# Kernel tuning notes

Hardware: AMD Instinct MI355X
Metric: run time of the kernel (lower is better)

The kernel has to match this reference:

```python
import jax, jax.numpy as jnp
import numpy as np

V, E, H, B, T = 32000, 256, 256, 4, 512


def setup_inputs() -> dict:
    key = jax.random.key(0)
    ks = jax.random.split(key, 16)
    s = 0.02
    d = {
        "x": jax.random.randint(ks[0], (B, T), 0, V, dtype=jnp.int64 if jax.config.read('jax_enable_x64') else jnp.int32).astype(jnp.int32),
        "h": jnp.zeros((1, B, H), jnp.float32),
        "embed_W": jax.random.normal(ks[1], (V, E), jnp.float32) * s,
        "gru_w_ih": jax.random.normal(ks[2], (3 * H, E), jnp.float32) * s,
        "gru_b_ih": jnp.zeros((3 * H,), jnp.float32),
        "gru_w_hh": jax.random.normal(ks[3], (3 * H, H), jnp.float32) * s,
        "gru_b_hh": jnp.zeros((3 * H,), jnp.float32),
        "attn_w_W": jax.random.normal(ks[4], (H, H), jnp.float32) * s,
        "attn_w_b": jnp.zeros((H,), jnp.float32),
        "attn_u_W": jax.random.normal(ks[5], (H, H), jnp.float32) * s,
        "attn_u_b": jnp.zeros((H,), jnp.float32),
        "attn_v_W": jax.random.normal(ks[6], (1, H), jnp.float32) * s,
        "attn_v_b": jnp.zeros((1,), jnp.float32),
        "fc_W": jax.random.normal(ks[7], (V, 2 * H), jnp.float32) * s,
        "fc_b": jnp.zeros((V,), jnp.float32),
    }
    return d


def reference(x, h, embed_W, gru_w_ih, gru_b_ih, gru_w_hh, gru_b_hh,
              attn_w_W, attn_w_b, attn_u_W, attn_u_b, attn_v_W, attn_v_b,
              fc_W, fc_b):
    # Embedding (dropout is identity in eval mode)
    emb = embed_W[x]                                   # [B,T,E]
    # GRU (single layer, batch_first), PyTorch gate math
    xp = emb @ gru_w_ih.T + gru_b_ih                   # [B,T,3H]
    h0 = h[0]                                          # [B,H]

    def step(hc, xpt):
        hp = hc @ gru_w_hh.T + gru_b_hh
        xr, xz, xn = jnp.split(xpt, 3, axis=-1)
        hr, hz, hn = jnp.split(hp, 3, axis=-1)
        r = jax.nn.sigmoid(xr + hr)
        z = jax.nn.sigmoid(xz + hz)
        n = jnp.tanh(xn + r * hn)
        h_new = (1.0 - z) * n + z * hc
        return h_new, h_new

    h_last, outs = jax.lax.scan(step, h0, jnp.swapaxes(xp, 0, 1))
    out = jnp.swapaxes(outs, 0, 1)                     # [B,T,H]

    # Bahdanau additive attention with causal mask
    q = out @ attn_w_W.T + attn_w_b                    # [B,T,H]
    k = out @ attn_u_W.T + attn_u_b                    # [B,T,H]
    e = jnp.tanh(q[:, :, None, :] + k[:, None, :, :])  # [B,T,T,H] (big intermediate)
    scores = jnp.einsum('bijh,h->bij', e, attn_v_W[0]) + attn_v_b[0]
    Tq = scores.shape[-1]
    causal_mask = jnp.triu(jnp.ones((Tq, Tq), bool), k=1)
    scores = jnp.where(causal_mask, -jnp.inf, scores)
    attn = jax.nn.softmax(scores, axis=-1)             # [B,T,T]
    ctx = jnp.einsum('bij,bjh->bih', attn, out)        # [B,T,H]

    combined = jnp.concatenate([out, ctx], axis=-1)    # [B,T,2H]
    logits = combined @ fc_W.T + fc_b                  # [B,T,V]
    return logits, h_last[None]
```

## Files before the change

kernel.cpp:

```cpp
#include <hip/hip_runtime.h>
#include <cstdint>
#include <cstddef>

#define Vv 32000
#define Ee 256
#define Hh 256
#define Bb 4
#define Tt 512
#define Mm (Bb*Tt)

typedef unsigned int u32;
typedef unsigned short u16;
typedef unsigned long long u64;
typedef __bf16 bf16x8 __attribute__((ext_vector_type(8)));
typedef float f32x4 __attribute__((ext_vector_type(4)));

__device__ __forceinline__ u16 f2bf(float f) {
  u32 u = __float_as_uint(f);
  u32 r = (u + 0x7FFFu + ((u >> 16) & 1u)) >> 16;
  return (u16)r;
}

template<bool GATHER>
__global__ __launch_bounds__(256) void gemm_small(
    const float* __restrict__ A, const int* __restrict__ xidx,
    const float* __restrict__ W, const float* __restrict__ bias,
    float* __restrict__ C, int N)
{
  __shared__ float At[64][36];
  __shared__ float Wt[64][66];
  const int tid = threadIdx.x;
  const int m0 = blockIdx.x * 32;
  const int n0 = blockIdx.y * 64;
  const int tm = tid >> 5;
  const int tn = tid & 31;
  float acc[4][2] = {};

  for (int k0 = 0; k0 < 256; k0 += 64) {
    __syncthreads();
    #pragma unroll
    for (int r = 0; r < 2; ++r) {
      int idx = tid + r*256;
      int i  = idx >> 4;
      int c4 = idx & 15;
      const float* src;
      if (GATHER) src = A + (size_t)xidx[m0+i]*256 + k0 + c4*4;
      else        src = A + (size_t)(m0+i)*256 + k0 + c4*4;
      float4 v = *(const float4*)src;
      At[c4*4+0][i]=v.x; At[c4*4+1][i]=v.y; At[c4*4+2][i]=v.z; At[c4*4+3][i]=v.w;
    }
    #pragma unroll
    for (int r = 0; r < 4; ++r) {
      int idx = tid + r*256;
      int j  = idx >> 4;
      int c4 = idx & 15;
      float4 v = *(const float4*)(W + (size_t)(n0+j)*256 + k0 + c4*4);
      Wt[c4*4+0][j]=v.x; Wt[c4*4+1][j]=v.y; Wt[c4*4+2][j]=v.z; Wt[c4*4+3][j]=v.w;
    }
    __syncthreads();
    #pragma unroll 8
    for (int k = 0; k < 64; ++k) {
      float4 a = *(const float4*)&At[k][tm*4];
      float2 w = *(const float2*)&Wt[k][tn*2];
      acc[0][0] += a.x*w.x; acc[0][1] += a.x*w.y;
      acc[1][0] += a.y*w.x; acc[1][1] += a.y*w.y;
      acc[2][0] += a.z*w.x; acc[2][1] += a.z*w.y;
      acc[3][0] += a.w*w.x; acc[3][1] += a.w*w.y;
    }
  }
  #pragma unroll
  for (int i = 0; i < 4; ++i)
    #pragma unroll
    for (int j = 0; j < 2; ++j) {
      int m = m0 + tm*4 + i, n = n0 + tn*2 + j;
      C[(size_t)m*N + n] = acc[i][j] + bias[n];
    }
}

__global__ __launch_bounds__(192, 1) void gru_scan(
    const float* __restrict__ xp, const float* __restrict__ h0,
    const float* __restrict__ whh, const float* __restrict__ bhh,
    float* __restrict__ gout, u64* __restrict__ hpair,
    const float* __restrict__ fcW, u16* __restrict__ Wb)
{
  const int tid = threadIdx.x;
  const int bid = blockIdx.x;
  const int b = bid & 7;
  const int c = bid >> 3;

  if (b >= 4) {
    const int cbid = (c << 2) | (b - 4);
    const int n8 = Vv*512/8;
    for (int i = cbid*192 + tid; i < n8; i += 32*192) {
      float4 a = ((const float4*)fcW)[i*2];
      float4 v = ((const float4*)fcW)[i*2+1];
      uint4 o;
      o.x = (u32)f2bf(a.x) | ((u32)f2bf(a.y) << 16);
      o.y = (u32)f2bf(a.z) | ((u32)f2bf(a.w) << 16);
      o.z = (u32)f2bf(v.x) | ((u32)f2bf(v.y) << 16);
      o.w = (u32)f2bf(v.z) | ((u32)f2bf(v.w) << 16);
      ((uint4*)Wb)[i] = o;
    }
    return;
  }

  __shared__ __attribute__((aligned(16))) float hl[256];
  __shared__ float dl[96];

  const int r = tid >> 1;
  const int q = tid & 1;
  const int grow = (r >> 5)*256 + c*32 + (r & 31);

  float w[128];
  {
    const f32x4* wp = (const f32x4*)(whh + (size_t)grow*256 + q*128);
    #pragma unroll
    for (int kk = 0; kk < 32; ++kk) {
      f32x4 v = wp[kk];
      w[4*kk+0] = v.x; w[4*kk+1] = v.y; w[4*kk+2] = v.z; w[4*kk+3] = v.w;
    }
  }
  #pragma unroll
  for (int kk = 0; kk < 128; ++kk) asm volatile("" : "+v"(w[kk]));

  float b_r = 0.f, b_z = 0.f, b_n = 0.f;
  const int jg = c*32 + (tid & 31);
  if (tid < 32) { b_r = bhh[jg]; b_z = bhh[256+jg]; b_n = bhh[512+jg]; }

  for (int t = 0; t < Tt; ++t) {
    float xr = 0.f, xz = 0.f, xn = 0.f;
    if (tid < 32) {
      size_t xb = ((size_t)(b*Tt) + t)*768 + jg;
      xr = xp[xb]; xz = xp[xb+256]; xn = xp[xb+512];
    }

    if (tid < 64) {
      float4 hv;
      if (t == 0) {
        hv = *(const float4*)(h0 + b*Hh + tid*4);
      } else {
        const u64* src = hpair + ((size_t)(b*2) + ((t-1)&1))*256 + tid*4;
        const u32 want = (u32)t;
        u64 v0, v1, v2, v3;
        for (;;) {
          v0 = __hip_atomic_load(src+0, __ATOMIC_RELAXED, __HIP_MEMORY_SCOPE_AGENT);
          v1 = __hip_atomic_load(src+1, __ATOMIC_RELAXED, __HIP_MEMORY_SCOPE_AGENT);
          v2 = __hip_atomic_load(src+2, __ATOMIC_RELAXED, __HIP_MEMORY_SCOPE_AGENT);
          v3 = __hip_atomic_load(src+3, __ATOMIC_RELAXED, __HIP_MEMORY_SCOPE_AGENT);
          if ((u32)(v0 >> 32) == want && (u32)(v1 >> 32) == want &&
              (u32)(v2 >> 32) == want && (u32)(v3 >> 32) == want) break;
        }
        hv.x = __uint_as_float((u32)v0); hv.y = __uint_as_float((u32)v1);
        hv.z = __uint_as_float((u32)v2); hv.w = __uint_as_float((u32)v3);
      }
      *(float4*)&hl[tid*4] = hv;
    }
    __syncthreads();

    float s0 = 0.f, s1 = 0.f, s2 = 0.f, s3 = 0.f;
    {
      const float* hp = &hl[q*128];
      #pragma unroll
      for (int kk = 0; kk < 32; ++kk) {
        float4 h4 = *(const float4*)(hp + kk*4);
        s0 += w[4*kk+0]*h4.x;
        s1 += w[4*kk+1]*h4.y;
        s2 += w[4*kk+2]*h4.z;
        s3 += w[4*kk+3]*h4.w;
      }
    }
    float s = (s0 + s1) + (s2 + s3);
    s += __shfl_xor(s, 1);
    if (q == 0) dl[r] = s;
    __syncthreads();

    if (tid < 32) {
      int j = tid;
      float dr = dl[j], dz = dl[32+j], dn = dl[64+j];
      float rr = 1.f/(1.f + __expf(-(xr + dr + b_r)));
      float zz = 1.f/(1.f + __expf(-(xz + dz + b_z)));
      float aa = xn + rr*(dn + b_n);
      float nn = 1.f - 2.f/(1.f + __expf(2.f*aa));
      float hp = hl[jg];
      float hn = (1.f - zz)*nn + zz*hp;
      u64 pv = ((u64)(u32)(t + 1) << 32) | (u64)__float_as_uint(hn);
      __hip_atomic_store(hpair + ((size_t)(b*2) + (t&1))*256 + jg, pv,
                         __ATOMIC_RELAXED, __HIP_MEMORY_SCOPE_AGENT);
      gout[((size_t)(b*Tt) + t)*Hh + jg] = hn;
    }
  }
}

__global__ __launch_bounds__(256) void attn_kernel(
    const float* __restrict__ outm, const float* __restrict__ qm,
    const float* __restrict__ km, const float* __restrict__ vW,
    const float* __restrict__ vb_p, float* __restrict__ ctx)
{
  __shared__ __attribute__((aligned(16))) float q[256];
  __shared__ __attribute__((aligned(16))) float vv[256];
  __shared__ float p[512];
  __shared__ float red[8];

  const int blk = blockIdx.x;
  const int b = blk >> 9;
  const int i = 511 - (blk & 511);
  const int tid = threadIdx.x;

  if (tid < 64) {
    ((float4*)q)[tid]  = ((const float4*)(qm + ((size_t)(b*Tt)+i)*Hh))[tid];
    ((float4*)vv)[tid] = ((const float4*)vW)[tid];
  }
  const float vb = vb_p[0];
  __syncthreads();

  for (int j = tid; j <= i; j += 256) {
    const float* kr = km + ((size_t)(b*Tt)+j)*Hh;
    float s = 0.f;
    #pragma unroll 4
    for (int h = 0; h < 256; h += 4) {
      float4 kv = *(const float4*)(kr + h);
      float x0 = q[h+0]+kv.x, x1 = q[h+1]+kv.y, x2 = q[h+2]+kv.z, x3 = q[h+3]+kv.w;
      s += vv[h+0]*(1.f - 2.f/(1.f + __expf(2.f*x0)));
      s += vv[h+1]*(1.f - 2.f/(1.f + __expf(2.f*x1)));
      s += vv[h+2]*(1.f - 2.f/(1.f + __expf(2.f*x2)));
      s += vv[h+3]*(1.f - 2.f/(1.f + __expf(2.f*x3)));
    }
    p[j] = s + vb;
  }
  __syncthreads();

  float m = -1e30f;
  for (int j = tid; j <= i; j += 256) m = fmaxf(m, p[j]);
  #pragma unroll
  for (int off = 32; off; off >>= 1) m = fmaxf(m, __shfl_xor(m, off));
  if ((tid & 63) == 0) red[tid >> 6] = m;
  __syncthreads();
  m = fmaxf(fmaxf(red[0], red[1]), fmaxf(red[2], red[3]));

  float s = 0.f;
  for (int j = tid; j <= i; j += 256) { float e = __expf(p[j]-m); p[j] = e; s += e; }
  #pragma unroll
  for (int off = 32; off; off >>= 1) s += __shfl_xor(s, off);
  if ((tid & 63) == 0) red[4 + (tid >> 6)] = s;
  __syncthreads();
  s = red[4]+red[5]+red[6]+red[7];
  const float inv = 1.f/s;

  float acc = 0.f;
  const float* op = outm + (size_t)(b*Tt)*Hh + tid;
  #pragma unroll 4
  for (int j = 0; j <= i; ++j) acc += p[j] * op[(size_t)j*Hh];
  ctx[((size_t)(b*Tt)+i)*Hh + tid] = acc*inv;
}

__global__ __launch_bounds__(256) void conv_comb_bf16(
    const float* __restrict__ gout, const float* __restrict__ ctx,
    u16* __restrict__ dst)
{
  int i = blockIdx.x*256 + threadIdx.x;
  int m  = i >> 6;
  int kg = (i & 63) * 8;
  const float* src = (kg < 256) ? (gout + (size_t)m*256 + kg)
                                : (ctx  + (size_t)m*256 + kg - 256);
  float4 a = *(const float4*)src;
  float4 b = *(const float4*)(src + 4);
  uint4 o;
  o.x = (u32)f2bf(a.x) | ((u32)f2bf(a.y) << 16);
  o.y = (u32)f2bf(a.z) | ((u32)f2bf(a.w) << 16);
  o.z = (u32)f2bf(b.x) | ((u32)f2bf(b.y) << 16);
  o.w = (u32)f2bf(b.z) | ((u32)f2bf(b.w) << 16);
  ((uint4*)dst)[i] = o;
}

__global__ __launch_bounds__(256) void fc_mfma(
    const u16* __restrict__ Ab, const u16* __restrict__ Wb,
    const float* __restrict__ bias, float* __restrict__ C)
{
  __shared__ __attribute__((aligned(16))) u16 As[128*32];
  __shared__ __attribute__((aligned(16))) u16 Bs[128*32];
  const int bid = blockIdx.x;
  const int mt = bid & 15, nt = bid >> 4;
  const int m0 = mt*128, n0 = nt*128;
  const int tid = threadIdx.x;
  const int wave = tid >> 6, lane = tid & 63;

  f32x4 acc[4][4];
  #pragma unroll
  for (int i = 0; i < 4; ++i)
    #pragma unroll
    for (int j = 0; j < 4; ++j)
      acc[i][j] = (f32x4){0.f, 0.f, 0.f, 0.f};

  const int wm = (wave & 1)*64;
  const int wn = (wave >> 1)*64;
  const int frow = lane & 15;
  const int fk   = (lane >> 4)*8;

  for (int k0 = 0; k0 < 512; k0 += 32) {
    __syncthreads();
    #pragma unroll
    for (int i = 0; i < 2; ++i) {
      int ebase = wave*1024 + i*512;
      int e = ebase + lane*8;
      int row = e >> 5, col = e & 31;
      __builtin_amdgcn_global_load_lds(
          (const __attribute__((address_space(1))) u32*)(Ab + (size_t)(m0+row)*512 + k0 + col),
          (__attribute__((address_space(3))) u32*)(As + ebase), 16, 0, 0);
      __builtin_amdgcn_global_load_lds(
          (const __attribute__((address_space(1))) u32*)(Wb + (size_t)(n0+row)*512 + k0 + col),
          (__attribute__((address_space(3))) u32*)(Bs + ebase), 16, 0, 0);
    }
    __syncthreads();

    bf16x8 af[4], bfr[4];
    #pragma unroll
    for (int mi = 0; mi < 4; ++mi)
      af[mi] = *(const bf16x8*)&As[(wm + mi*16 + frow)*32 + fk];
    #pragma unroll
    for (int ni = 0; ni < 4; ++ni)
      bfr[ni] = *(const bf16x8*)&Bs[(wn + ni*16 + frow)*32 + fk];
    #pragma unroll
    for (int mi = 0; mi < 4; ++mi)
      #pragma unroll
      for (int ni = 0; ni < 4; ++ni)
        acc[mi][ni] = __builtin_amdgcn_mfma_f32_16x16x32_bf16(af[mi], bfr[ni], acc[mi][ni], 0, 0, 0);
  }

  const int coln = lane & 15, rq = (lane >> 4)*4;
  #pragma unroll
  for (int ni = 0; ni < 4; ++ni) {
    int n = n0 + wn + ni*16 + coln;
    float bb = bias[n];
    #pragma unroll
    for (int mi = 0; mi < 4; ++mi) {
      int mbase = m0 + wm + mi*16 + rq;
      #pragma unroll
      for (int r2 = 0; r2 < 4; ++r2)
        C[(size_t)(mbase + r2)*Vv + n] = acc[mi][ni][r2] + bb;
    }
  }
}

__global__ void copy_hlast(const float* __restrict__ gout, float* __restrict__ dst)
{
  int idx = blockIdx.x*256 + threadIdx.x;
  if (idx < Bb*Hh) {
    int b = idx >> 8, h = idx & 255;
    dst[idx] = gout[((size_t)(b*Tt) + (Tt-1))*Hh + h];
  }
}

extern "C" void kernel_launch(void* const* d_in, const int* in_sizes, int n_in,
                              void* d_out, int out_size, void* d_ws, size_t ws_size,
                              hipStream_t stream)
{
  const int*   x    = (const int*)  d_in[0];
  const float* h0   = (const float*)d_in[1];
  const float* embW = (const float*)d_in[2];
  const float* wih  = (const float*)d_in[3];
  const float* bih  = (const float*)d_in[4];
  const float* whh  = (const float*)d_in[5];
  const float* bhh  = (const float*)d_in[6];
  const float* awW  = (const float*)d_in[7];
  const float* awb  = (const float*)d_in[8];
  const float* auW  = (const float*)d_in[9];
  const float* aub  = (const float*)d_in[10];
  const float* avW  = (const float*)d_in[11];
  const float* avb  = (const float*)d_in[12];
  const float* fcW  = (const float*)d_in[13];
  const float* fcb  = (const float*)d_in[14];
  float* outp = (float*)d_out;

  float* ws   = (float*)d_ws;
  float* xp   = ws;
  float* gout = xp   + (size_t)Mm*768;
  float* q    = gout + (size_t)Mm*Hh;
  float* k    = q    + (size_t)Mm*Hh;
  float* ctx  = k    + (size_t)Mm*Hh;
  u64*  hpair = (u64*)(ctx + (size_t)Mm*Hh);
  u16* comb = (u16*)(hpair + 2048);
  u16* Wb   = comb + (size_t)Mm*512;

  dim3 g1(Mm/32, 768/64);
  gemm_small<true><<<g1, 256, 0, stream>>>(embW, x, wih, bih, xp, 768);

  gru_scan<<<64, 192, 0, stream>>>(xp, h0, whh, bhh, gout, hpair, fcW, Wb);

  dim3 g3(Mm/32, 256/64);
  gemm_small<false><<<g3, 256, 0, stream>>>(gout, nullptr, awW, awb, q, 256);
  gemm_small<false><<<g3, 256, 0, stream>>>(gout, nullptr, auW, aub, k, 256);

  attn_kernel<<<Bb*Tt, 256, 0, stream>>>(gout, q, k, avW, avb, ctx);

  conv_comb_bf16<<<512, 256, 0, stream>>>(gout, ctx, comb);

  fc_mfma<<<16*250, 256, 0, stream>>>(comb, Wb, fcb, outp);

  copy_hlast<<<4, 256, 0, stream>>>(gout, outp + (size_t)Mm*Vv);
}
```

Measured before the change: 1.375 ms.

## Restructure GRU scan: 512 threads, shuffle reductions, LDS flag sync, 4-slot exchange

Rebuilds the recurrent GRU kernel around 512 threads per block. Each group of 16 lanes now owns one hidden unit and holds its r/z/n weight slices in registers, and partial dot products are combined with xor shuffles instead of a shared-memory pass. The two __syncthreads per step are replaced by an acquire spin on a double-buffered LDS tag, and the inter-block h exchange buffer grows from 2 to 4 slots and is zeroed by a memset before launch. The aim is to shorten the per-timestep critical path of the serial scan, at the cost of lane-level spinning and more threads on the side blocks that convert the FC weights to bf16.

```diff
diff --git a/kernel.cpp b/kernel.cpp
--- a/kernel.cpp
+++ b/kernel.cpp
@@ -77,7 +77,7 @@
     }
 }
 
-__global__ __launch_bounds__(192, 1) void gru_scan(
+__global__ __launch_bounds__(512, 1) void gru_scan(
     const float* __restrict__ xp, const float* __restrict__ h0,
     const float* __restrict__ whh, const float* __restrict__ bhh,
     float* __restrict__ gout, u64* __restrict__ hpair,
@@ -91,7 +91,7 @@
   if (b >= 4) {
     const int cbid = (c << 2) | (b - 4);
     const int n8 = Vv*512/8;
-    for (int i = cbid*192 + tid; i < n8; i += 32*192) {
+    for (int i = cbid*512 + tid; i < n8; i += 32*512) {
       float4 a = ((const float4*)fcW)[i*2];
       float4 v = ((const float4*)fcW)[i*2+1];
       uint4 o;
@@ -104,33 +104,40 @@
     return;
   }
 
-  __shared__ __attribute__((aligned(16))) float hl[256];
-  __shared__ float dl[96];
-
-  const int r = tid >> 1;
-  const int q = tid & 1;
-  const int grow = (r >> 5)*256 + c*32 + (r & 31);
-
-  float w[128];
+  __shared__ __attribute__((aligned(16))) float hl[2][256];
+  __shared__ u32 htag[2];
+
+  const int j = tid >> 4;
+  const int g = tid & 15;
+
+  if (tid < 2) htag[tid] = 0;
+  __syncthreads();
+
+  float w[48];
   {
-    const f32x4* wp = (const f32x4*)(whh + (size_t)grow*256 + q*128);
-    #pragma unroll
-    for (int kk = 0; kk < 32; ++kk) {
-      f32x4 v = wp[kk];
-      w[4*kk+0] = v.x; w[4*kk+1] = v.y; w[4*kk+2] = v.z; w[4*kk+3] = v.w;
-    }
-  }
-  #pragma unroll
-  for (int kk = 0; kk < 128; ++kk) asm volatile("" : "+v"(w[kk]));
-
-  float b_r = 0.f, b_z = 0.f, b_n = 0.f;
-  const int jg = c*32 + (tid & 31);
-  if (tid < 32) { b_r = bhh[jg]; b_z = bhh[256+jg]; b_n = bhh[512+jg]; }
+    #pragma unroll
+    for (int m = 0; m < 4; ++m) {
+      float4 vr = *(const float4*)(whh + (size_t)(      c*32 + j)*256 + g*4 + 64*m);
+      float4 vz = *(const float4*)(whh + (size_t)(256 + c*32 + j)*256 + g*4 + 64*m);
+      float4 vn = *(const float4*)(whh + (size_t)(512 + c*32 + j)*256 + g*4 + 64*m);
+      w[   m*4+0]=vr.x; w[   m*4+1]=vr.y; w[   m*4+2]=vr.z; w[   m*4+3]=vr.w;
+      w[16+m*4+0]=vz.x; w[16+m*4+1]=vz.y; w[16+m*4+2]=vz.z; w[16+m*4+3]=vz.w;
+      w[32+m*4+0]=vn.x; w[32+m*4+1]=vn.y; w[32+m*4+2]=vn.z; w[32+m*4+3]=vn.w;
+    }
+  }
+  #pragma unroll
+  for (int kk = 0; kk < 48; ++kk) asm volatile("" : "+v"(w[kk]));
+
+  float b_r = 0.f, b_z = 0.f, b_n = 0.f, hprev = 0.f;
+  if (g == 0) {
+    b_r = bhh[c*32 + j]; b_z = bhh[256 + c*32 + j]; b_n = bhh[512 + c*32 + j];
+    hprev = h0[b*Hh + c*32 + j];
+  }
 
   for (int t = 0; t < Tt; ++t) {
     float xr = 0.f, xz = 0.f, xn = 0.f;
-    if (tid < 32) {
-      size_t xb = ((size_t)(b*Tt) + t)*768 + jg;
+    if (g == 0) {
+      size_t xb = ((size_t)(b*Tt) + t)*768 + c*32 + j;
       xr = xp[xb]; xz = xp[xb+256]; xn = xp[xb+512];
     }
 
@@ -139,54 +146,56 @@
       if (t == 0) {
         hv = *(const float4*)(h0 + b*Hh + tid*4);
       } else {
-        const u64* src = hpair + ((size_t)(b*2) + ((t-1)&1))*256 + tid*4;
+        const u64* src = hpair + ((size_t)(b*4) + ((t-1)&3))*256 + tid*4;
         const u32 want = (u32)t;
-        u64 v0, v1, v2, v3;
         for (;;) {
-          v0 = __hip_atomic_load(src+0, __ATOMIC_RELAXED, __HIP_MEMORY_SCOPE_AGENT);
-          v1 = __hip_atomic_load(src+1, __ATOMIC_RELAXED, __HIP_MEMORY_SCOPE_AGENT);
-          v2 = __hip_atomic_load(src+2, __ATOMIC_RELAXED, __HIP_MEMORY_SCOPE_AGENT);
-          v3 = __hip_atomic_load(src+3, __ATOMIC_RELAXED, __HIP_MEMORY_SCOPE_AGENT);
-          if ((u32)(v0 >> 32) == want && (u32)(v1 >> 32) == want &&
-              (u32)(v2 >> 32) == want && (u32)(v3 >> 32) == want) break;
+          u64 v0 = __hip_atomic_load(src+0, __ATOMIC_RELAXED, __HIP_MEMORY_SCOPE_AGENT);
+          u64 v1 = __hip_atomic_load(src+1, __ATOMIC_RELAXED, __HIP_MEMORY_SCOPE_AGENT);
+          u64 v2 = __hip_atomic_load(src+2, __ATOMIC_RELAXED, __HIP_MEMORY_SCOPE_AGENT);
+          u64 v3 = __hip_atomic_load(src+3, __ATOMIC_RELAXED, __HIP_MEMORY_SCOPE_AGENT);
+          if (((u32)(v0 >> 32) == want) & ((u32)(v1 >> 32) == want) &
+              ((u32)(v2 >> 32) == want) & ((u32)(v3 >> 32) == want)) {
+            hv.x = __uint_as_float((u32)v0); hv.y = __uint_as_float((u32)v1);
+            hv.z = __uint_as_float((u32)v2); hv.w = __uint_as_float((u32)v3);
+            break;
+          }
         }
-        hv.x = __uint_as_float((u32)v0); hv.y = __uint_as_float((u32)v1);
-        hv.z = __uint_as_float((u32)v2); hv.w = __uint_as_float((u32)v3);
       }
-      *(float4*)&hl[tid*4] = hv;
-    }
-    __syncthreads();
-
-    float s0 = 0.f, s1 = 0.f, s2 = 0.f, s3 = 0.f;
-    {
-      const float* hp = &hl[q*128];
-      #pragma unroll
-      for (int kk = 0; kk < 32; ++kk) {
-        float4 h4 = *(const float4*)(hp + kk*4);
-        s0 += w[4*kk+0]*h4.x;
-        s1 += w[4*kk+1]*h4.y;
-        s2 += w[4*kk+2]*h4.z;
-        s3 += w[4*kk+3]*h4.w;
-      }
-    }
-    float s = (s0 + s1) + (s2 + s3);
-    s += __shfl_xor(s, 1);
-    if (q == 0) dl[r] = s;
-    __syncthreads();
-
-    if (tid < 32) {
-      int j = tid;
-      float dr = dl[j], dz = dl[32+j], dn = dl[64+j];
-      float rr = 1.f/(1.f + __expf(-(xr + dr + b_r)));
-      float zz = 1.f/(1.f + __expf(-(xz + dz + b_z)));
-      float aa = xn + rr*(dn + b_n);
+      *(float4*)&hl[t&1][tid*4] = hv;
+      if (tid == 0)
+        __hip_atomic_store(&htag[t&1], (u32)(t+1),
+                           __ATOMIC_RELEASE, __HIP_MEMORY_SCOPE_WORKGROUP);
+    }
+
+    while (__hip_atomic_load(&htag[t&1], __ATOMIC_ACQUIRE,
+                             __HIP_MEMORY_SCOPE_WORKGROUP) != (u32)(t+1)) {}
+
+    float sr = 0.f, sz = 0.f, sn = 0.f;
+    #pragma unroll
+    for (int m = 0; m < 4; ++m) {
+      float4 h4 = *(const float4*)&hl[t&1][g*4 + 64*m];
+      sr += w[   m*4+0]*h4.x + w[   m*4+1]*h4.y + w[   m*4+2]*h4.z + w[   m*4+3]*h4.w;
+      sz += w[16+m*4+0]*h4.x + w[16+m*4+1]*h4.y + w[16+m*4+2]*h4.z + w[16+m*4+3]*h4.w;
+      sn += w[32+m*4+0]*h4.x + w[32+m*4+1]*h4.y + w[32+m*4+2]*h4.z + w[32+m*4+3]*h4.w;
+    }
+    #pragma unroll
+    for (int d = 1; d < 16; d <<= 1) {
+      sr += __shfl_xor(sr, d);
+      sz += __shfl_xor(sz, d);
+      sn += __shfl_xor(sn, d);
+    }
+
+    if (g == 0) {
+      float rr = 1.f/(1.f + __expf(-(xr + sr + b_r)));
+      float zz = 1.f/(1.f + __expf(-(xz + sz + b_z)));
+      float aa = xn + rr*(sn + b_n);
       float nn = 1.f - 2.f/(1.f + __expf(2.f*aa));
-      float hp = hl[jg];
-      float hn = (1.f - zz)*nn + zz*hp;
+      float hn = (1.f - zz)*nn + zz*hprev;
       u64 pv = ((u64)(u32)(t + 1) << 32) | (u64)__float_as_uint(hn);
-      __hip_atomic_store(hpair + ((size_t)(b*2) + (t&1))*256 + jg, pv,
+      __hip_atomic_store(hpair + ((size_t)(b*4) + (t&3))*256 + c*32 + j, pv,
                          __ATOMIC_RELAXED, __HIP_MEMORY_SCOPE_AGENT);
-      gout[((size_t)(b*Tt) + t)*Hh + jg] = hn;
+      gout[((size_t)(b*Tt) + t)*Hh + c*32 + j] = hn;
+      hprev = hn;
     }
   }
 }
@@ -378,13 +387,15 @@
   float* k    = q    + (size_t)Mm*Hh;
   float* ctx  = k    + (size_t)Mm*Hh;
   u64*  hpair = (u64*)(ctx + (size_t)Mm*Hh);
-  u16* comb = (u16*)(hpair + 2048);
+  u16* comb = (u16*)(hpair + 4096);
   u16* Wb   = comb + (size_t)Mm*512;
+
+  hipMemsetAsync(hpair, 0, 4096*sizeof(u64), stream);
 
   dim3 g1(Mm/32, 768/64);
   gemm_small<true><<<g1, 256, 0, stream>>>(embW, x, wih, bih, xp, 768);
 
-  gru_scan<<<64, 192, 0, stream>>>(xp, h0, whh, bhh, gout, hpair, fcW, Wb);
+  gru_scan<<<64, 512, 0, stream>>>(xp, h0, whh, bhh, gout, hpair, fcW, Wb);
 
   dim3 g3(Mm/32, 256/64);
   gemm_small<false><<<g3, 256, 0, stream>>>(gout, nullptr, awW, awb, q, 256);
```

New measurement: 1.262 ms. -8.2%, faster.
